# Performance work log

Hardware: AMD Instinct MI355X
Metric: run time of the kernel (lower is better)

Reference implementation:

```python
import jax, jax.numpy as jnp
import numpy as np

E = 512
H = 8
D = E // H  # head_dims = 64
MAXREL = 512


def setup_inputs() -> dict:
    key = jax.random.key(0)
    ks = jax.random.split(key, 12)
    B, L = 4, 1024
    s_lin = float(np.sqrt(6.0 / (D + D)))  # xavier uniform for (D,D)
    s_fc = float(np.sqrt(6.0 / (E + E)))
    s_tab = float(np.sqrt(6.0 / (2 * MAXREL + 1 + D)))
    return {
        "query": jax.random.normal(ks[0], (B, L, E), jnp.float32),
        "key": jax.random.normal(ks[1], (B, L, E), jnp.float32),
        "value": jax.random.normal(ks[2], (B, L, E), jnp.float32),
        "mask": jax.random.randint(ks[3], (B, 1, 1, L), 0, 2, jnp.int32),
        "Wq": jax.random.uniform(ks[4], (D, D), jnp.float32, -s_lin, s_lin),
        "bq": jnp.zeros((D,), jnp.float32),
        "Wk": jax.random.uniform(ks[5], (D, D), jnp.float32, -s_lin, s_lin),
        "bk": jnp.zeros((D,), jnp.float32),
        "Wv": jax.random.uniform(ks[6], (D, D), jnp.float32, -s_lin, s_lin),
        "bv": jnp.zeros((D,), jnp.float32),
        "Wfc": jax.random.uniform(ks[7], (E, E), jnp.float32, -s_fc, s_fc),
        "bfc": jnp.zeros((E,), jnp.float32),
        "rel_k_table": jax.random.uniform(ks[8], (2 * MAXREL + 1, D), jnp.float32, -s_tab, s_tab),
        "rel_v_table": jax.random.uniform(ks[9], (2 * MAXREL + 1, D), jnp.float32, -s_tab, s_tab),
    }


def _rel_indices(length_q, length_k):
    dist = jnp.arange(length_k)[None, :] - jnp.arange(length_q)[:, None]
    return jnp.clip(dist, -MAXREL, MAXREL) + MAXREL  # [Q, K]


def reference(query, key, value, mask, Wq, bq, Wk, bk, Wv, bv, Wfc, bfc, rel_k_table, rel_v_table):
    B, Q, _ = query.shape
    K = key.shape[1]
    q = query.reshape(B, Q, H, D) @ Wq.T + bq  # per-head linear (same weights all heads)
    k = key.reshape(B, K, H, D) @ Wk.T + bk
    v = value.reshape(B, K, H, D) @ Wv.T + bv

    scores = jnp.einsum("bqhd,bkhd->bhqk", q, k)  # [B,H,Q,K]
    scores = jnp.where(mask == 0, jnp.float32(-1e20), scores)  # mask BEFORE bias & scale, as in source

    idx = _rel_indices(Q, K)
    a_key = rel_k_table[idx]    # [Q,K,D]
    a_val = rel_v_table[idx]    # [Q,K,D]
    scores = scores + jnp.einsum("bqhd,qkd->bhqk", q, a_key)

    attn = jax.nn.softmax(scores / jnp.sqrt(jnp.float32(D)), axis=-1)

    out = jnp.einsum("bhqk,bkhd->bqhd", attn, v)  # standard AV
    out = out + jnp.einsum("bhqk,qkd->bqhd", attn, a_val)  # relative-position value term
    out = out.reshape(B, Q, H * D)
    return out @ Wfc.T + bfc
```

## Files before the change

kernel.cpp:

```cpp
#include <hip/hip_runtime.h>
#include <math.h>

#define BB 4
#define LL 1024
#define EE 512
#define HH 8
#define DD 64
#define MAXREL 512

typedef unsigned short u16;
typedef __attribute__((ext_vector_type(8))) short bf16x8;
typedef __attribute__((ext_vector_type(4))) float f32x4;

__device__ __forceinline__ u16 f2bf(float f) {
    unsigned int u = __float_as_uint(f);
    unsigned int r = (u + 0x7FFFu + ((u >> 16) & 1u)) >> 16;
    return (u16)r;
}
__device__ __forceinline__ bf16x8 ldf8_bf(const float* p) {
    const float4 a = *(const float4*)(p);
    const float4 b = *(const float4*)(p + 4);
    bf16x8 r;
    r[0] = (short)f2bf(a.x); r[1] = (short)f2bf(a.y);
    r[2] = (short)f2bf(a.z); r[3] = (short)f2bf(a.w);
    r[4] = (short)f2bf(b.x); r[5] = (short)f2bf(b.y);
    r[6] = (short)f2bf(b.z); r[7] = (short)f2bf(b.w);
    return r;
}

#define MF(A, B, C) __builtin_amdgcn_mfma_f32_16x16x32_bf16((A), (B), (C), 0, 0, 0)
#define EXPSC 0.1803368801111244f

__global__ __launch_bounds__(256) void proj_mfma_kernel(
    const float* __restrict__ q_in, const float* __restrict__ k_in, const float* __restrict__ v_in,
    const float* __restrict__ Wq, const float* __restrict__ bq,
    const float* __restrict__ Wk, const float* __restrict__ bk,
    const float* __restrict__ Wv, const float* __restrict__ bv,
    u16* __restrict__ qb, u16* __restrict__ kb, u16* __restrict__ vtb)
{
    int bh = blockIdx.x; int b = bh >> 3; int h = bh & 7;
    int l0 = blockIdx.y * 64;
    int t = threadIdx.x; int w = t >> 6; int lane = t & 63;
    int lg = lane >> 4, lc = lane & 15;
    int lt = l0 + w * 16;

    bf16x8 wq[4][2], wk[4][2], wv[4][2];
    #pragma unroll
    for (int dt = 0; dt < 4; ++dt)
        #pragma unroll
        for (int kc = 0; kc < 2; ++kc) {
            int d = dt * 16 + lc, ko = kc * 32 + lg * 8;
            wq[dt][kc] = ldf8_bf(Wq + d * DD + ko);
            wk[dt][kc] = ldf8_bf(Wk + d * DD + ko);
            wv[dt][kc] = ldf8_bf(Wv + d * DD + ko);
        }
    size_t xrow = ((size_t)b * LL + lt + lc) * EE + h * DD;
    bf16x8 xq[2], xk[2], xv[2];
    #pragma unroll
    for (int kc = 0; kc < 2; ++kc) {
        int ko = kc * 32 + lg * 8;
        xq[kc] = ldf8_bf(q_in + xrow + ko);
        xk[kc] = ldf8_bf(k_in + xrow + ko);
        xv[kc] = ldf8_bf(v_in + xrow + ko);
    }

    f32x4 aq[4] = {}, ak[4] = {}, av[4] = {};
    #pragma unroll
    for (int dt = 0; dt < 4; ++dt) {
        aq[dt] = MF(wq[dt][0], xq[0], aq[dt]);
        aq[dt] = MF(wq[dt][1], xq[1], aq[dt]);
        ak[dt] = MF(wk[dt][0], xk[0], ak[dt]);
        ak[dt] = MF(wk[dt][1], xk[1], ak[dt]);
        av[dt] = MF(xv[0], wv[dt][0], av[dt]);
        av[dt] = MF(xv[1], wv[dt][1], av[dt]);
    }

    #pragma unroll
    for (int dt = 0; dt < 4; ++dt) {
        u16 tq[4], tk[4], tv[4];
        #pragma unroll
        for (int r = 0; r < 4; ++r) {
            int d = dt * 16 + lg * 4 + r;
            tq[r] = f2bf(aq[dt][r] + bq[d]);
            tk[r] = f2bf(ak[dt][r] + bk[d]);
            tv[r] = f2bf(av[dt][r] + bv[dt * 16 + lc]);
        }
        size_t o = ((size_t)bh * LL + lt + lc) * DD + dt * 16 + lg * 4;
        *(uint2*)&qb[o] = *(uint2*)tq;
        *(uint2*)&kb[o] = *(uint2*)tk;
        size_t ov = ((size_t)bh * DD + dt * 16 + lc) * LL + lt + lg * 4;
        *(uint2*)&vtb[ov] = *(uint2*)tv;
    }
}

__global__ __launch_bounds__(256) void prep_kernel(
    const float* __restrict__ relk, const float* __restrict__ relv, const float* __restrict__ Wfc,
    u16* __restrict__ relk_pad, u16* __restrict__ relvt_pad, u16* __restrict__ wfcb)
{
    int idx = blockIdx.x * 256 + threadIdx.x;
    if (idx < 2048 * DD) {
        int r = idx >> 6, d = idx & 63;
        int j = r - 512; j = j < 0 ? 0 : (j > 2 * MAXREL ? 2 * MAXREL : j);
        relk_pad[idx] = f2bf(relk[j * DD + d]);
        int dd = idx >> 11, c = idx & 2047;
        int j2 = c - 512; j2 = j2 < 0 ? 0 : (j2 > 2 * MAXREL ? 2 * MAXREL : j2);
        relvt_pad[idx] = f2bf(relv[j2 * DD + dd]);
    }
    if (idx < EE * EE) wfcb[idx] = f2bf(Wfc[idx]);
}

__global__ __launch_bounds__(256) void attn_mfma_kernel(
    const u16* __restrict__ qb, const u16* __restrict__ kb, const u16* __restrict__ vtb,
    const int* __restrict__ mask,
    const u16* __restrict__ relk_pad, const u16* __restrict__ relvt_pad,
    u16* __restrict__ attn_out)
{
    __shared__ __align__(16) char smem[48384];
    u16* Ks   = (u16*)(smem);
    u16* Vts  = (u16*)(smem + 9216);
    u16* RVts = (u16*)(smem + 18432);
    float* lred = (float*)(smem + 48128);
    float* obuf = (float*)smem;

    int bh = blockIdx.x, b = bh >> 3, h = bh & 7;
    int q0 = blockIdx.y * 32;
    int t = threadIdx.x, lane = t & 63, w = t >> 6;
    int rw = w & 1, cw = w >> 1;
    int rbase = rw * 16, c0a = cw * 32;
    int lg = lane >> 4, lc = lane & 15;
    int ub = c0a - rbase + 16;
    size_t bhL = (size_t)bh * LL;
    const u16* kb_bh = kb + bhL * DD;
    const u16* vt_bh = vtb + (size_t)bh * DD * LL;
    const int* mk_b = mask + b * LL;
    u16* Pw  = (u16*)(smem + 33792) + w * 640;
    u16* Pqw = (u16*)(smem + 38912) + w * 1152;

    int sr0 = t >> 3, ss0 = (t & 7) * 8;
    int sr1 = sr0 + 32;
    int rv_row = t >> 2, rv_q = (t & 3) * 24;
    const u16* rvg = relvt_pad + (size_t)rv_row * 2048 + rv_q;
    u16* rvl = RVts + rv_row * 120 + rv_q;
    const u16* rk_base = relk_pad + (size_t)(ub + lc) * DD + lg * 8;

    const u16* qrow = qb + (bhL + q0 + rbase + lc) * DD;
    bf16x8 qf0 = *(const bf16x8*)&qrow[lg * 8];
    bf16x8 qf1 = *(const bf16x8*)&qrow[32 + lg * 8];

    f32x4 s0, s1, g0, g1, g2;
    bf16x8 rk0, rk1, rk2, rk3, rk4, rk5;
    f32x4 oacc[4] = {};
    float lacc[4] = {0.f, 0.f, 0.f, 0.f};
    int delta0 = lc - lg * 4;

#define LOAD_RK(SB) do { \
    const u16* rkp_ = rk_base + (size_t)(SB) * DD; \
    rk0 = *(const bf16x8*)&rkp_[0]; \
    rk1 = *(const bf16x8*)&rkp_[32]; \
    rk2 = *(const bf16x8*)&rkp_[16 * DD]; \
    rk3 = *(const bf16x8*)&rkp_[16 * DD + 32]; \
    rk4 = *(const bf16x8*)&rkp_[32 * DD]; \
    rk5 = *(const bf16x8*)&rkp_[32 * DD + 32]; \
} while (0)

#define DO_SCORES() do { \
    const u16* kp0_ = Ks + (c0a + lc) * 72; \
    const u16* kp1_ = Ks + (c0a + 16 + lc) * 72; \
    s0 = (f32x4){0.f,0.f,0.f,0.f}; s1 = s0; g0 = s0; g1 = s0; g2 = s0; \
    __builtin_amdgcn_s_setprio(1); \
    s0 = MF(qf0, *(const bf16x8*)&kp0_[lg * 8], s0); \
    s0 = MF(qf1, *(const bf16x8*)&kp0_[32 + lg * 8], s0); \
    s1 = MF(qf0, *(const bf16x8*)&kp1_[lg * 8], s1); \
    s1 = MF(qf1, *(const bf16x8*)&kp1_[32 + lg * 8], s1); \
    g0 = MF(qf0, rk0, g0); g0 = MF(qf1, rk1, g0); \
    g1 = MF(qf0, rk2, g1); g1 = MF(qf1, rk3, g1); \
    g2 = MF(qf0, rk4, g2); g2 = MF(qf1, rk5, g2); \
    __builtin_amdgcn_s_setprio(0); \
} while (0)

#define DO_SOFTMAX(MB0, MB1) do { \
    _Pragma("unroll") \
    for (int r = 0; r < 4; ++r) { \
        int d_ = delta0 - r; \
        int src_ = (lane & 48) | (d_ & 15); \
        float a0_ = __shfl(g0[r], src_, 64); \
        float a1_ = __shfl(g1[r], src_, 64); \
        float a2_ = __shfl(g2[r], src_, 64); \
        float gv0_ = (d_ >= 0) ? a1_ : a0_; \
        float gv1_ = (d_ >= 0) ? a2_ : a1_; \
        float p0_ = exp2f((s0[r] + (MB0) + gv0_) * EXPSC); \
        float p1_ = exp2f((s1[r] + (MB1) + gv1_) * EXPSC); \
        unsigned pk_; \
        asm("v_cvt_pk_bf16_f32 %0, %1, %2" : "=v"(pk_) : "v"(p0_), "v"(p1_)); \
        u16 pb0_ = (u16)pk_, pb1_ = (u16)(pk_ >> 16); \
        lacc[r] += p0_ + p1_; \
        int row_ = lg * 4 + r; \
        Pw[row_ * 40 + lc] = pb0_; \
        Pw[row_ * 40 + 16 + lc] = pb1_; \
        Pqw[row_ * 72 + lc - row_ + 16] = pb0_; \
        Pqw[row_ * 72 + 32 + lc - row_] = pb1_; \
    } \
} while (0)

    #pragma unroll
    for (int i = 0; i < 3; ++i) {
        int u = lane + i * 64;
        if (u < 144) *(uint4*)&Pqw[u * 8] = make_uint4(0, 0, 0, 0);
    }
    if (t < 192) {
        int row = t / 3, j = t - row * 3;
        *(uint4*)&RVts[row * 120 + 96 + j * 8] = make_uint4(0, 0, 0, 0);
    }
    int sb0 = 992 - q0;
    *(uint4*)&Ks[sr0 * 72 + ss0] = *(const uint4*)&kb_bh[(size_t)sr0 * DD + ss0];
    *(uint4*)&Ks[sr1 * 72 + ss0] = *(const uint4*)&kb_bh[(size_t)sr1 * DD + ss0];
    *(uint4*)&Vts[sr0 * 72 + ss0] = *(const uint4*)&vt_bh[(size_t)sr0 * LL + ss0];
    *(uint4*)&Vts[sr1 * 72 + ss0] = *(const uint4*)&vt_bh[(size_t)sr1 * LL + ss0];
    *(uint4*)&rvl[0]  = *(const uint4*)&rvg[sb0];
    *(uint4*)&rvl[8]  = *(const uint4*)&rvg[sb0 + 8];
    *(uint4*)&rvl[16] = *(const uint4*)&rvg[sb0 + 16];
    LOAD_RK(sb0);
    float mbp0 = (mk_b[c0a + lc] != 0) ? 0.f : -1e20f;
    float mbp1 = (mk_b[c0a + 16 + lc] != 0) ? 0.f : -1e20f;
    __syncthreads();
    DO_SCORES();
    LOAD_RK(sb0 + 64);
    DO_SOFTMAX(mbp0, mbp1);
    {
        uint4 k1a = *(const uint4*)&kb_bh[(size_t)(64 + sr0) * DD + ss0];
        uint4 k1b = *(const uint4*)&kb_bh[(size_t)(64 + sr1) * DD + ss0];
        __syncthreads();
        *(uint4*)&Ks[sr0 * 72 + ss0] = k1a;
        *(uint4*)&Ks[sr1 * 72 + ss0] = k1b;
        __syncthreads();
    }

    #pragma unroll 1
    for (int c = 0; c < 16; ++c) {
        int k0 = c * 64;
        int sb_ = k0 - q0 + 992;
        uint4 rK0, rK1, rV0, rV1, rRV0, rRV1, rRV2;
        float mbn0 = 0.f, mbn1 = 0.f;
        if (c < 14) {
            rK0 = *(const uint4*)&kb_bh[(size_t)(k0 + 128 + sr0) * DD + ss0];
            rK1 = *(const uint4*)&kb_bh[(size_t)(k0 + 128 + sr1) * DD + ss0];
        }
        if (c < 15) {
            int k0n = k0 + 64;
            int sbn = sb_ + 64;
            rV0  = *(const uint4*)&vt_bh[(size_t)sr0 * LL + k0n + ss0];
            rV1  = *(const uint4*)&vt_bh[(size_t)sr1 * LL + k0n + ss0];
            rRV0 = *(const uint4*)&rvg[sbn];
            rRV1 = *(const uint4*)&rvg[sbn + 8];
            rRV2 = *(const uint4*)&rvg[sbn + 16];
            mbn0 = (mk_b[k0n + c0a + lc] != 0) ? 0.f : -1e20f;
            mbn1 = (mk_b[k0n + c0a + 16 + lc] != 0) ? 0.f : -1e20f;
        }

        bf16x8 pa  = *(const bf16x8*)&Pw[lc * 40 + lg * 8];
        bf16x8 pq0 = *(const bf16x8*)&Pqw[lc * 72 + lg * 8];
        bf16x8 pq1 = *(const bf16x8*)&Pqw[lc * 72 + 32 + lg * 8];

        if (c < 15) {
            DO_SCORES();
            if (c < 14) LOAD_RK(sb_ + 128);
        }

        __builtin_amdgcn_s_setprio(1);
        #pragma unroll
        for (int dt = 0; dt < 4; ++dt) {
            const u16* vp = &Vts[(dt * 16 + lc) * 72 + c0a];
            const u16* rp = &RVts[(dt * 16 + lc) * 120 + ub];
            oacc[dt] = MF(pa,  *(const bf16x8*)&vp[lg * 8], oacc[dt]);
            oacc[dt] = MF(pq0, *(const bf16x8*)&rp[lg * 8], oacc[dt]);
            oacc[dt] = MF(pq1, *(const bf16x8*)&rp[32 + lg * 8], oacc[dt]);
        }
        __builtin_amdgcn_s_setprio(0);

        if (c < 15) {
            DO_SOFTMAX(mbn0, mbn1);
            __syncthreads();
            if (c < 14) {
                *(uint4*)&Ks[sr0 * 72 + ss0] = rK0;
                *(uint4*)&Ks[sr1 * 72 + ss0] = rK1;
            }
            *(uint4*)&Vts[sr0 * 72 + ss0] = rV0;
            *(uint4*)&Vts[sr1 * 72 + ss0] = rV1;
            *(uint4*)&rvl[0]  = rRV0;
            *(uint4*)&rvl[8]  = rRV1;
            *(uint4*)&rvl[16] = rRV2;
            __syncthreads();
        }
    }
#undef LOAD_RK
#undef DO_SCORES
#undef DO_SOFTMAX

    #pragma unroll
    for (int m2 = 1; m2 <= 8; m2 <<= 1) {
        #pragma unroll
        for (int r = 0; r < 4; ++r) lacc[r] += __shfl_xor(lacc[r], m2);
    }
    __syncthreads();
    if (lc == 0) {
        #pragma unroll
        for (int r = 0; r < 4; ++r) lred[cw * 32 + rbase + lg * 4 + r] = lacc[r];
    }
    __syncthreads();
    if (cw == 1) {
        #pragma unroll
        for (int dt = 0; dt < 4; ++dt)
            #pragma unroll
            for (int r = 0; r < 4; ++r)
                obuf[(rbase + lg * 4 + r) * 68 + dt * 16 + lc] = oacc[dt][r];
    }
    __syncthreads();
    if (cw == 0) {
        float inv[4];
        #pragma unroll
        for (int r = 0; r < 4; ++r) {
            int row = rbase + lg * 4 + r;
            inv[r] = 1.0f / (lred[row] + lred[32 + row]);
        }
        #pragma unroll
        for (int dt = 0; dt < 4; ++dt) {
            #pragma unroll
            for (int r = 0; r < 4; ++r) {
                int row = rbase + lg * 4 + r;
                float v = (oacc[dt][r] + obuf[row * 68 + dt * 16 + lc]) * inv[r];
                attn_out[((size_t)b * LL + q0 + row) * EE + h * DD + dt * 16 + lc] = f2bf(v);
            }
        }
    }
}

__global__ __launch_bounds__(256) void fc_mfma_kernel(
    const u16* __restrict__ Xb, const u16* __restrict__ Wb,
    const float* __restrict__ bfc, float* __restrict__ out)
{
    __shared__ u16 As[128][72];
    __shared__ u16 Bs[128][72];
    int m0 = blockIdx.x * 128, n0 = blockIdx.y * 128;
    int t = threadIdx.x, lane = t & 63, w = t >> 6;
    int rw = w & 1, cw = w >> 1;
    int lg = lane >> 4, lc = lane & 15;
    f32x4 acc[4][4] = {};

    for (int kt = 0; kt < EE; kt += 64) {
        __syncthreads();
        #pragma unroll
        for (int i = 0; i < 4; ++i) {
            int unit = i * 256 + t;
            int row = unit >> 3, s = unit & 7;
            *(uint4*)&As[row][s * 8] = *(const uint4*)&Xb[(size_t)(m0 + row) * EE + kt + s * 8];
            *(uint4*)&Bs[row][s * 8] = *(const uint4*)&Wb[(size_t)(n0 + row) * EE + kt + s * 8];
        }
        __syncthreads();
        #pragma unroll
        for (int kc = 0; kc < 2; ++kc) {
            bf16x8 af[4], bf[4];
            #pragma unroll
            for (int i = 0; i < 4; ++i) {
                af[i] = *(const bf16x8*)&As[rw * 64 + i * 16 + lc][kc * 32 + lg * 8];
                bf[i] = *(const bf16x8*)&Bs[cw * 64 + i * 16 + lc][kc * 32 + lg * 8];
            }
            #pragma unroll
            for (int mi = 0; mi < 4; ++mi)
                #pragma unroll
                for (int ni = 0; ni < 4; ++ni)
                    acc[mi][ni] = MF(af[mi], bf[ni], acc[mi][ni]);
        }
    }
    #pragma unroll
    for (int mi = 0; mi < 4; ++mi) {
        #pragma unroll
        for (int ni = 0; ni < 4; ++ni) {
            int n = n0 + cw * 64 + ni * 16 + lc;
            float bias = bfc[n];
            #pragma unroll
            for (int r = 0; r < 4; ++r) {
                int m = m0 + rw * 64 + mi * 16 + lg * 4 + r;
                out[(size_t)m * EE + n] = acc[mi][ni][r] + bias;
            }
        }
    }
}

extern "C" void kernel_launch(void* const* d_in, const int* in_sizes, int n_in,
                              void* d_out, int out_size, void* d_ws, size_t ws_size,
                              hipStream_t stream) {
    const float* query = (const float*)d_in[0];
    const float* key   = (const float*)d_in[1];
    const float* value = (const float*)d_in[2];
    const int*   mask  = (const int*)d_in[3];
    const float* Wq  = (const float*)d_in[4];
    const float* bq  = (const float*)d_in[5];
    const float* Wk  = (const float*)d_in[6];
    const float* bk  = (const float*)d_in[7];
    const float* Wv  = (const float*)d_in[8];
    const float* bv  = (const float*)d_in[9];
    const float* Wfc = (const float*)d_in[10];
    const float* bfc = (const float*)d_in[11];
    const float* relk = (const float*)d_in[12];
    const float* relv = (const float*)d_in[13];
    float* out = (float*)d_out;

    char* ws = (char*)d_ws;
    u16* qb        = (u16*)(ws);
    u16* kb        = (u16*)(ws + (4u << 20));
    u16* vtb       = (u16*)(ws + (8u << 20));
    u16* attnb     = (u16*)(ws + (12u << 20));
    u16* relk_pad  = (u16*)(ws + (16u << 20));
    u16* relvt_pad = (u16*)(ws + (16u << 20) + 262144);
    u16* wfcb      = (u16*)(ws + (16u << 20) + 524288);

    proj_mfma_kernel<<<dim3(BB * HH, LL / 64), 256, 0, stream>>>(
        query, key, value, Wq, bq, Wk, bk, Wv, bv, qb, kb, vtb);
    prep_kernel<<<1024, 256, 0, stream>>>(relk, relv, Wfc, relk_pad, relvt_pad, wfcb);
    attn_mfma_kernel<<<dim3(BB * HH, LL / 32), 256, 0, stream>>>(
        qb, kb, vtb, mask, relk_pad, relvt_pad, attnb);
    fc_mfma_kernel<<<dim3(BB * LL / 128, EE / 128), 256, 0, stream>>>(attnb, wfcb, bfc, out);
}
```

Measured before the change: 108.2 us.

## Switch PV accumulation to 32x32x16 MFMA with block-shared P tiles

The P·V and relative-value products now use 32x32x16 bf16 MFMAs. Each wave owns a 32-row by 32-dim output tile and splits the key range across waves by row-half, instead of running 16x16 tiles per wave. P and its shifted copy are written to block-wide shared buffers, and the fragments are read after the barrier. The relative-value table is re-laid out with a wider padded stride so a 48-column window per row-half can be fetched. The intent is to cut MFMA instruction count and the redundant V/RV LDS reads, at the cost of an extra cross-wave dependency on P through shared memory and a changed epilogue reduction.

```diff
diff --git a/kernel.cpp b/kernel.cpp
--- a/kernel.cpp
+++ b/kernel.cpp
@@ -11,6 +11,7 @@
 typedef unsigned short u16;
 typedef __attribute__((ext_vector_type(8))) short bf16x8;
 typedef __attribute__((ext_vector_type(4))) float f32x4;
+typedef __attribute__((ext_vector_type(16))) float f32x16;
 
 __device__ __forceinline__ u16 f2bf(float f) {
     unsigned int u = __float_as_uint(f);
@@ -28,7 +29,8 @@
     return r;
 }
 
-#define MF(A, B, C) __builtin_amdgcn_mfma_f32_16x16x32_bf16((A), (B), (C), 0, 0, 0)
+#define MF(A, B, C)   __builtin_amdgcn_mfma_f32_16x16x32_bf16((A), (B), (C), 0, 0, 0)
+#define MF32(A, B, C) __builtin_amdgcn_mfma_f32_32x32x16_bf16((A), (B), (C), 0, 0, 0)
 #define EXPSC 0.1803368801111244f
 
 __global__ __launch_bounds__(256) void proj_mfma_kernel(
@@ -95,16 +97,19 @@
 
 __global__ __launch_bounds__(256) void prep_kernel(
     const float* __restrict__ relk, const float* __restrict__ relv, const float* __restrict__ Wfc,
-    u16* __restrict__ relk_pad, u16* __restrict__ relvt_pad, u16* __restrict__ wfcb)
+    u16* __restrict__ relk_pad, u16* __restrict__ relvt2, u16* __restrict__ wfcb)
 {
     int idx = blockIdx.x * 256 + threadIdx.x;
     if (idx < 2048 * DD) {
         int r = idx >> 6, d = idx & 63;
         int j = r - 512; j = j < 0 ? 0 : (j > 2 * MAXREL ? 2 * MAXREL : j);
         relk_pad[idx] = f2bf(relk[j * DD + d]);
-        int dd = idx >> 11, c = idx & 2047;
-        int j2 = c - 512; j2 = j2 < 0 ? 0 : (j2 > 2 * MAXREL ? 2 * MAXREL : j2);
-        relvt_pad[idx] = f2bf(relv[j2 * DD + dd]);
+    }
+    if (idx < DD * 3072) {
+        int d = idx / 3072;
+        int c = idx - d * 3072;
+        int j = c - 512; j = j < 0 ? 0 : (j > 2 * MAXREL ? 2 * MAXREL : j);
+        relvt2[idx] = f2bf(relv[j * DD + d]);
     }
     if (idx < EE * EE) wfcb[idx] = f2bf(Wfc[idx]);
 }
@@ -112,14 +117,16 @@
 __global__ __launch_bounds__(256) void attn_mfma_kernel(
     const u16* __restrict__ qb, const u16* __restrict__ kb, const u16* __restrict__ vtb,
     const int* __restrict__ mask,
-    const u16* __restrict__ relk_pad, const u16* __restrict__ relvt_pad,
+    const u16* __restrict__ relk_pad, const u16* __restrict__ relvt2,
     u16* __restrict__ attn_out)
 {
-    __shared__ __align__(16) char smem[48384];
+    __shared__ __align__(16) char smem[45312];
     u16* Ks   = (u16*)(smem);
     u16* Vts  = (u16*)(smem + 9216);
     u16* RVts = (u16*)(smem + 18432);
-    float* lred = (float*)(smem + 48128);
+    u16* Ps   = (u16*)(smem + 33792);
+    u16* Pqs  = (u16*)(smem + 38400);
+    float* lred = (float*)(smem + 45056);
     float* obuf = (float*)smem;
 
     int bh = blockIdx.x, b = bh >> 3, h = bh & 7;
@@ -129,17 +136,16 @@
     int rbase = rw * 16, c0a = cw * 32;
     int lg = lane >> 4, lc = lane & 15;
     int ub = c0a - rbase + 16;
+    int m_ = lane & 31, h8 = (lane >> 5) * 8, hh = (lane >> 5) * 4;
     size_t bhL = (size_t)bh * LL;
     const u16* kb_bh = kb + bhL * DD;
     const u16* vt_bh = vtb + (size_t)bh * DD * LL;
     const int* mk_b = mask + b * LL;
-    u16* Pw  = (u16*)(smem + 33792) + w * 640;
-    u16* Pqw = (u16*)(smem + 38912) + w * 1152;
 
     int sr0 = t >> 3, ss0 = (t & 7) * 8;
     int sr1 = sr0 + 32;
     int rv_row = t >> 2, rv_q = (t & 3) * 24;
-    const u16* rvg = relvt_pad + (size_t)rv_row * 2048 + rv_q;
+    const u16* rvg = relvt2 + (size_t)rv_row * 3072 + rv_q;
     u16* rvl = RVts + rv_row * 120 + rv_q;
     const u16* rk_base = relk_pad + (size_t)(ub + lc) * DD + lg * 8;
 
@@ -149,7 +155,8 @@
 
     f32x4 s0, s1, g0, g1, g2;
     bf16x8 rk0, rk1, rk2, rk3, rk4, rk5;
-    f32x4 oacc[4] = {};
+    bf16x8 pa0, pa1, pr0, pr1, pr2;
+    f32x16 oacc = {};
     float lacc[4] = {0.f, 0.f, 0.f, 0.f};
     int delta0 = lc - lg * 4;
 
@@ -194,23 +201,23 @@
         asm("v_cvt_pk_bf16_f32 %0, %1, %2" : "=v"(pk_) : "v"(p0_), "v"(p1_)); \
         u16 pb0_ = (u16)pk_, pb1_ = (u16)(pk_ >> 16); \
         lacc[r] += p0_ + p1_; \
-        int row_ = lg * 4 + r; \
-        Pw[row_ * 40 + lc] = pb0_; \
-        Pw[row_ * 40 + 16 + lc] = pb1_; \
-        Pqw[row_ * 72 + lc - row_ + 16] = pb0_; \
-        Pqw[row_ * 72 + 32 + lc - row_] = pb1_; \
+        int row_ = rbase + lg * 4 + r; \
+        Ps[row_ * 72 + c0a + lc] = pb0_; \
+        Ps[row_ * 72 + c0a + 16 + lc] = pb1_; \
+        Pqs[row_ * 104 + c0a + lc - row_ + 32] = pb0_; \
+        Pqs[row_ * 104 + c0a + 16 + lc - row_ + 32] = pb1_; \
     } \
 } while (0)
 
-    #pragma unroll
-    for (int i = 0; i < 3; ++i) {
-        int u = lane + i * 64;
-        if (u < 144) *(uint4*)&Pqw[u * 8] = make_uint4(0, 0, 0, 0);
-    }
-    if (t < 192) {
-        int row = t / 3, j = t - row * 3;
-        *(uint4*)&RVts[row * 120 + 96 + j * 8] = make_uint4(0, 0, 0, 0);
-    }
+#define READ_PFRAGS() do { \
+    pa0 = *(const bf16x8*)&Ps[m_ * 72 + rw * 32 + h8]; \
+    pa1 = *(const bf16x8*)&Ps[m_ * 72 + rw * 32 + 16 + h8]; \
+    pr0 = *(const bf16x8*)&Pqs[m_ * 104 + rw * 48 + h8]; \
+    pr1 = *(const bf16x8*)&Pqs[m_ * 104 + rw * 48 + 16 + h8]; \
+    pr2 = *(const bf16x8*)&Pqs[m_ * 104 + rw * 48 + 32 + h8]; \
+} while (0)
+
+    for (int i = t; i < 416; i += 256) ((uint4*)Pqs)[i] = make_uint4(0, 0, 0, 0);
     int sb0 = 992 - q0;
     *(uint4*)&Ks[sr0 * 72 + ss0] = *(const uint4*)&kb_bh[(size_t)sr0 * DD + ss0];
     *(uint4*)&Ks[sr1 * 72 + ss0] = *(const uint4*)&kb_bh[(size_t)sr1 * DD + ss0];
@@ -232,6 +239,7 @@
         __syncthreads();
         *(uint4*)&Ks[sr0 * 72 + ss0] = k1a;
         *(uint4*)&Ks[sr1 * 72 + ss0] = k1b;
+        READ_PFRAGS();
         __syncthreads();
     }
 
@@ -257,23 +265,20 @@
             mbn1 = (mk_b[k0n + c0a + 16 + lc] != 0) ? 0.f : -1e20f;
         }
 
-        bf16x8 pa  = *(const bf16x8*)&Pw[lc * 40 + lg * 8];
-        bf16x8 pq0 = *(const bf16x8*)&Pqw[lc * 72 + lg * 8];
-        bf16x8 pq1 = *(const bf16x8*)&Pqw[lc * 72 + 32 + lg * 8];
-
         if (c < 15) {
             DO_SCORES();
             if (c < 14) LOAD_RK(sb_ + 128);
         }
 
         __builtin_amdgcn_s_setprio(1);
-        #pragma unroll
-        for (int dt = 0; dt < 4; ++dt) {
-            const u16* vp = &Vts[(dt * 16 + lc) * 72 + c0a];
-            const u16* rp = &RVts[(dt * 16 + lc) * 120 + ub];
-            oacc[dt] = MF(pa,  *(const bf16x8*)&vp[lg * 8], oacc[dt]);
-            oacc[dt] = MF(pq0, *(const bf16x8*)&rp[lg * 8], oacc[dt]);
-            oacc[dt] = MF(pq1, *(const bf16x8*)&rp[32 + lg * 8], oacc[dt]);
+        {
+            const u16* vrow = &Vts[(cw * 32 + m_) * 72 + rw * 32];
+            const u16* rrow = &RVts[(cw * 32 + m_) * 120 + rw * 48];
+            oacc = MF32(pa0, *(const bf16x8*)&vrow[h8], oacc);
+            oacc = MF32(pa1, *(const bf16x8*)&vrow[16 + h8], oacc);
+            oacc = MF32(pr0, *(const bf16x8*)&rrow[h8], oacc);
+            oacc = MF32(pr1, *(const bf16x8*)&rrow[16 + h8], oacc);
+            oacc = MF32(pr2, *(const bf16x8*)&rrow[32 + h8], oacc);
         }
         __builtin_amdgcn_s_setprio(0);
 
@@ -289,12 +294,14 @@
             *(uint4*)&rvl[0]  = rRV0;
             *(uint4*)&rvl[8]  = rRV1;
             *(uint4*)&rvl[16] = rRV2;
+            READ_PFRAGS();
             __syncthreads();
         }
     }
 #undef LOAD_RK
 #undef DO_SCORES
 #undef DO_SOFTMAX
+#undef READ_PFRAGS
 
     #pragma unroll
     for (int m2 = 1; m2 <= 8; m2 <<= 1) {
@@ -307,29 +314,20 @@
         for (int r = 0; r < 4; ++r) lred[cw * 32 + rbase + lg * 4 + r] = lacc[r];
     }
     __syncthreads();
-    if (cw == 1) {
-        #pragma unroll
-        for (int dt = 0; dt < 4; ++dt)
-            #pragma unroll
-            for (int r = 0; r < 4; ++r)
-                obuf[(rbase + lg * 4 + r) * 68 + dt * 16 + lc] = oacc[dt][r];
+    if (rw == 1) {
+        #pragma unroll
+        for (int reg = 0; reg < 16; ++reg) {
+            int row = (reg & 3) + 8 * (reg >> 2) + hh;
+            obuf[row * 68 + cw * 32 + m_] = oacc[reg];
+        }
     }
     __syncthreads();
-    if (cw == 0) {
-        float inv[4];
-        #pragma unroll
-        for (int r = 0; r < 4; ++r) {
-            int row = rbase + lg * 4 + r;
-            inv[r] = 1.0f / (lred[row] + lred[32 + row]);
-        }
-        #pragma unroll
-        for (int dt = 0; dt < 4; ++dt) {
-            #pragma unroll
-            for (int r = 0; r < 4; ++r) {
-                int row = rbase + lg * 4 + r;
-                float v = (oacc[dt][r] + obuf[row * 68 + dt * 16 + lc]) * inv[r];
-                attn_out[((size_t)b * LL + q0 + row) * EE + h * DD + dt * 16 + lc] = f2bf(v);
-            }
+    if (rw == 0) {
+        #pragma unroll
+        for (int reg = 0; reg < 16; ++reg) {
+            int row = (reg & 3) + 8 * (reg >> 2) + hh;
+            float v = (oacc[reg] + obuf[row * 68 + cw * 32 + m_]) / (lred[row] + lred[32 + row]);
+            attn_out[((size_t)b * LL + q0 + row) * EE + h * DD + cw * 32 + m_] = f2bf(v);
         }
     }
 }
@@ -411,13 +409,13 @@
     u16* vtb       = (u16*)(ws + (8u << 20));
     u16* attnb     = (u16*)(ws + (12u << 20));
     u16* relk_pad  = (u16*)(ws + (16u << 20));
-    u16* relvt_pad = (u16*)(ws + (16u << 20) + 262144);
-    u16* wfcb      = (u16*)(ws + (16u << 20) + 524288);
+    u16* relvt2    = (u16*)(ws + (16u << 20) + 262144);
+    u16* wfcb      = (u16*)(ws + (16u << 20) + 655360);
 
     proj_mfma_kernel<<<dim3(BB * HH, LL / 64), 256, 0, stream>>>(
         query, key, value, Wq, bq, Wk, bk, Wv, bv, qb, kb, vtb);
-    prep_kernel<<<1024, 256, 0, stream>>>(relk, relv, Wfc, relk_pad, relvt_pad, wfcb);
+    prep_kernel<<<1024, 256, 0, stream>>>(relk, relv, Wfc, relk_pad, relvt2, wfcb);
     attn_mfma_kernel<<<dim3(BB * HH, LL / 32), 256, 0, stream>>>(
-        qb, kb, vtb, mask, relk_pad, relvt_pad, attnb);
+        qb, kb, vtb, mask, relk_pad, relvt2, attnb);
     fc_mfma_kernel<<<dim3(BB * LL / 128, EE / 128), 256, 0, stream>>>(attnb, wfcb, bfc, out);
 }
```

After: 107.2 us. No clear change (-0.9%).
